# Kernel optimization log

Measured on AMD Instinct MI355X. Metric: run time of the kernel, lower is better.

The kernel has to match this reference:

```python
import jax, jax.numpy as jnp
import numpy as np

E = 32  # embedding_dim
B = 1048576

def setup_inputs() -> dict:
    key = jax.random.key(0)
    ks = jax.random.split(key, 16)
    def p(k, shape, scale=0.1):
        return jax.random.normal(k, shape, dtype=jnp.float32) * scale
    return {
        'x': jax.random.normal(ks[0], (B, 2, 5), dtype=jnp.float32),
        'fc_emb_w': p(ks[1], (E, 5)), 'fc_emb_b': p(ks[2], (E,)),
        'in_proj_w': p(ks[3], (3 * E, E)), 'in_proj_b': p(ks[4], (3 * E,)),
        'out_proj_w': p(ks[5], (E, E)), 'out_proj_b': p(ks[6], (E,)),
        'w_ih': p(ks[7], (E, E)), 'b_ih': p(ks[8], (E,)),
        'w_hh': p(ks[9], (E, E)), 'b_hh': p(ks[10], (E,)),
        'fc_dec_w': p(ks[11], (5, E)), 'fc_dec_b': p(ks[12], (5,)),
        'out_w': p(ks[13], (3, 5)), 'out_b': p(ks[14], (3,)),
    }

def gelu(x):
    return jax.nn.gelu(x, approximate=False)  # torch nn.GELU default (erf)

def reference(x, fc_emb_w, fc_emb_b, in_proj_w, in_proj_b,
              out_proj_w, out_proj_b, w_ih, b_ih, w_hh, b_hh,
              fc_dec_w, fc_dec_b, out_w, out_b):
    # per-token embedding: [B,2,5] -> [B,2,E]
    e = gelu(jnp.einsum('bsi,ei->bse', x, fc_emb_w) + fc_emb_b)
    # single-head self-attention (seq_len=2)
    wq, wk, wv = jnp.split(in_proj_w, 3, axis=0)
    bq, bk, bv = jnp.split(in_proj_b, 3, axis=0)
    q = jnp.einsum('bsd,ed->bse', e, wq) + bq
    k = jnp.einsum('bsd,ed->bse', e, wk) + bk
    v = jnp.einsum('bsd,ed->bse', e, wv) + bv
    scores = jnp.einsum('bqd,bkd->bqk', q, k) / jnp.sqrt(jnp.float32(E))
    attn = jax.nn.softmax(scores, axis=-1)
    o = jnp.einsum('bqk,bkd->bqd', attn, v)
    o = jnp.einsum('bsd,ed->bse', o, out_proj_w) + out_proj_b
    # 2-step tanh RNN, h0 = 0; final hidden state only
    h1 = jnp.tanh(o[:, 0] @ w_ih.T + b_ih + b_hh)
    h2 = jnp.tanh(o[:, 1] @ w_ih.T + b_ih + h1 @ w_hh.T + b_hh)
    # decode
    d = gelu(h2 @ fc_dec_w.T + fc_dec_b)
    return d @ out_w.T + out_b  # [B,3]
```

## Files before the change

kernel.cpp:

```cpp
#include <hip/hip_runtime.h>
#include <math.h>

#define BT 256

typedef _Float16 half2v __attribute__((ext_vector_type(2)));
typedef __fp16   fp16x2 __attribute__((ext_vector_type(2)));
typedef _Float16 half8  __attribute__((ext_vector_type(8)));
typedef float    f32x16 __attribute__((ext_vector_type(16)));

union U4H8 { unsigned int u[4]; half8 h; };
struct __attribute__((packed)) F3 { float a, b, c; };

__device__ __forceinline__ half2v u2h(unsigned int u){
  union { unsigned int u; half2v h; } c; c.u = u; return c.h;
}
__device__ __forceinline__ unsigned int h2u(half2v h){
  union { unsigned int u; half2v h; } c; c.h = h; return c.u;
}
__device__ __forceinline__ half2v pkrtz(float a, float b){
  union { fp16x2 f; half2v h; } c;
  c.f = __builtin_amdgcn_cvt_pkrtz(a, b);
  return c.h;
}
__device__ __forceinline__ float fdot2(half2v a, half2v b, float c){
  return __builtin_amdgcn_fdot2(a, b, c, false);
}
__device__ __forceinline__ float frcp(float x){ return __builtin_amdgcn_rcpf(x); }

__device__ __forceinline__ unsigned int pk_rne(float a, float b){
  half2v h; h.x = (_Float16)a; h.y = (_Float16)b; return h2u(h);
}

#if __has_builtin(__builtin_amdgcn_permlane32_swap)
#define HAVE_PLSWAP 1
#endif

__device__ __forceinline__ float red_sum32(float v){
#ifdef HAVE_PLSWAP
  union { float f; unsigned u; } c; c.f = v;
  auto r = __builtin_amdgcn_permlane32_swap(c.u, c.u, false, false);
  union { unsigned u; float f; } a, b; a.u = r[0]; b.u = r[1];
  return a.f + b.f;
#else
  return v + __shfl_xor(v, 32);
#endif
}
__device__ __forceinline__ float upper_to_lower(float v){
#ifdef HAVE_PLSWAP
  union { float f; unsigned u; } c; c.f = v;
  auto r = __builtin_amdgcn_permlane32_swap(c.u, c.u, false, false);
  union { unsigned u; float f; } b; b.u = r[1];
  return b.f;
#else
  return __shfl_xor(v, 32);
#endif
}
__device__ __forceinline__ float lower_to_upper(float v){
#ifdef HAVE_PLSWAP
  union { float f; unsigned u; } c; c.f = v;
  auto r = __builtin_amdgcn_permlane32_swap(c.u, c.u, false, false);
  union { unsigned u; float f; } a; a.u = r[0];
  return a.f;
#else
  return __shfl_xor(v, 32);
#endif
}

__device__ __forceinline__ half2v gelu_pk(half2v x){
  const _Float16 a0 = (_Float16)0.3989423f,  a1 = (_Float16)-0.0663157f,
                 a2 = (_Float16)0.0096298f,  a3 = (_Float16)-0.00095967f,
                 a4 = (_Float16)0.000048f,   hp = (_Float16)0.5f,
                 hn = (_Float16)-0.5f;
  const half2v A0={a0,a0}, A1={a1,a1}, A2={a2,a2}, A3={a3,a3}, A4={a4,a4};
  const half2v HP={hp,hp}, HN={hn,hn};
  half2v t = x*x;
  half2v q = A4*t + A3;
  q = q*t + A2;
  q = q*t + A1;
  q = q*t + A0;
  half2v u = x*q;
#if __has_builtin(__builtin_elementwise_min)
  u = __builtin_elementwise_max(u, HN);
  u = __builtin_elementwise_min(u, HP);
#else
  u.x = u.x > hp ? hp : (u.x < hn ? hn : u.x);
  u.y = u.y > hp ? hp : (u.y < hn ? hn : u.y);
#endif
  return x*(u + HP);
}

__device__ __forceinline__ half2v tanh_pk(half2v x){
  const _Float16 c0=(_Float16)0.999716f,  c1=(_Float16)-0.328107f,
                 c2=(_Float16)0.116352f,  c3=(_Float16)-0.031255f,
                 c4=(_Float16)0.005038f,  c5=(_Float16)-0.000348f,
                 tp=(_Float16)2.0f,       tn=(_Float16)-2.0f;
  const half2v C0={c0,c0},C1={c1,c1},C2={c2,c2},C3={c3,c3},C4={c4,c4},C5={c5,c5};
  const half2v TP={tp,tp}, TN={tn,tn};
#if __has_builtin(__builtin_elementwise_min)
  x = __builtin_elementwise_max(x, TN);
  x = __builtin_elementwise_min(x, TP);
#else
  x.x = x.x > tp ? tp : (x.x < tn ? tn : x.x);
  x.y = x.y > tp ? tp : (x.y < tn ? tn : x.y);
#endif
  half2v t = x*x;
  half2v p = C5*t + C4;
  p = p*t + C3;
  p = p*t + C2;
  p = p*t + C1;
  p = p*t + C0;
  return x*p;
}

__global__ void prep_kernel(const float* __restrict__ inw, const float* __restrict__ inb,
                            const float* __restrict__ opw, const float* __restrict__ opb,
                            const float* __restrict__ wih, const float* __restrict__ bih,
                            const float* __restrict__ bhh, const float* __restrict__ whh,
                            const float* __restrict__ decw, const float* __restrict__ embw,
                            const float* __restrict__ embb,
                            const float* __restrict__ decb, const float* __restrict__ outw,
                            unsigned int* __restrict__ wsu){
  __shared__ float sQ[1024], sK[1024], sV[1024], sOP[1024], sWI[1024];
  __shared__ float sA[1024], sP[1024], sM[1024], sT[32], sWV[32];
  const float ISS = 0.17677669529663689f;
  int t = threadIdx.x;
  sQ[t]  = inw[t];
  sK[t]  = inw[1024 + t];
  sV[t]  = inw[2048 + t];
  sOP[t] = opw[t];
  sWI[t] = wih[t];
  __syncthreads();
  int tx = t & 31, ty = t >> 5;
  float accA = 0.f, accP = 0.f;
  #pragma unroll
  for (int m = 0; m < 32; m++){
    accA += sQ[m*32 + ty] * sK[m*32 + tx];
    accP += sOP[ty*32 + m] * sV[m*32 + tx];
  }
  sA[ty*32 + tx] = accA;
  sP[ty*32 + tx] = accP;
  if (ty == 0){
    float aw = 0.f;
    #pragma unroll
    for (int m = 0; m < 32; m++) aw += inb[m] * sK[m*32 + tx];
    sWV[tx] = aw;
  }
  if (ty == 1){
    float at = opb[tx];
    #pragma unroll
    for (int m = 0; m < 32; m++) at += sOP[tx*32 + m] * inb[64 + m];
    sT[tx] = at;
  }
  __syncthreads();
  float accM = 0.f;
  #pragma unroll
  for (int m = 0; m < 32; m++) accM += sWI[ty*32 + m] * sP[m*32 + tx];
  sM[ty*32 + tx] = accM;
  if (ty == 2){
    float ab = bih[tx] + bhh[tx];
    #pragma unroll
    for (int m = 0; m < 32; m++) ab += sWI[tx*32 + m] * sT[m];
    ((float*)wsu)[2320 + tx] = ab;
  }
  __syncthreads();
  if (t < 512){
    int r = t >> 4, j = t & 15;
    int c0 = 16*(j>>3) + 8*((j>>1)&1) + 4*((j>>2)&1) + 2*(j&1);
    wsu[t]        = pk_rne(ISS*sA[r*32+c0], ISS*sA[r*32+c0+1]);
    wsu[512 + t]  = pk_rne(sM[r*32+c0],  sM[r*32+c0+1]);
    wsu[1024 + t] = pk_rne(whh[r*32+c0], whh[r*32+c0+1]);
    wsu[1536 + t] = (r < 5) ? pk_rne(decw[r*32+c0], decw[r*32+c0+1]) : 0u;
  } else if (t < 768){
    int q = t - 512, j2 = q >> 3, cc = (q & 7)*2;
    float a = (cc   < 5) ? embw[j2*5+cc]   : 0.f;
    float b = (cc+1 < 5) ? embw[j2*5+cc+1] : ((cc+1 == 5) ? embb[j2] : 0.f);
    wsu[2048 + q] = pk_rne(a, b);
  } else if (t < 784){
    int q = t - 768, gg = q >> 3, j = q & 7;
    int r0 = 2*(j&1) + 8*(j>>1) + 4*gg;
    wsu[2304 + q] = pk_rne(ISS*sWV[r0], ISS*sWV[r0+1]);
  } else if (t < 787){
    int i = t - 784, c = 2*i;
    float a = decb[c];
    float b = (c+1 < 5) ? decb[c+1] : 0.f;
    wsu[2352 + i] = pk_rne(a, b);
  } else if (t < 796){
    int q = t - 787;
    int r = (q >= 6) ? 2 : ((q >= 3) ? 1 : 0);
    int p = q - r*3, c = 2*p;
    float a = outw[r*5 + c];
    float b = (c+1 < 5) ? outw[r*5 + c + 1] : 0.f;
    wsu[2355 + q] = pk_rne(a, b);
  }
}

__device__ __forceinline__ half8 ldfrag(const unsigned int* __restrict__ p){
  U4H8 t; t.u[0]=p[0]; t.u[1]=p[1]; t.u[2]=p[2]; t.u[3]=p[3]; return t.h;
}
__device__ __forceinline__ half8 h8of(const unsigned int* q){
  U4H8 t; t.u[0]=q[0]; t.u[1]=q[1]; t.u[2]=q[2]; t.u[3]=q[3]; return t.h;
}

__device__ __forceinline__ f32x16 ldbias(const float* __restrict__ p, int grp){
  const float4* b = (const float4*)(p + 4*grp);
  float4 q0 = b[0], q1 = b[2], q2 = b[4], q3 = b[6];
  f32x16 c;
  c[0]=q0.x; c[1]=q0.y; c[2]=q0.z; c[3]=q0.w;
  c[4]=q1.x; c[5]=q1.y; c[6]=q1.z; c[7]=q1.w;
  c[8]=q2.x; c[9]=q2.y; c[10]=q2.z; c[11]=q2.w;
  c[12]=q3.x; c[13]=q3.y; c[14]=q3.z; c[15]=q3.w;
  return c;
}

__global__ __launch_bounds__(BT, 4) void fused_kernel(
    const float* __restrict__ x,
    const unsigned int* __restrict__ wsu,
    const float* __restrict__ outb,
    float* __restrict__ y, long long B)
{
  int tid  = threadIdx.x;
  int lane = tid & 63;
  int col  = lane & 31;
  bool g   = (lane >> 5) != 0;
  int grp  = g ? 1 : 0;

  unsigned B32  = (unsigned)B;
  unsigned Bm1  = B32 - 1u;
  unsigned eBase = ((unsigned)blockIdx.x*(BT/64) + (unsigned)(tid>>6)) * 64u;
  if (eBase >= B32) return;
  bool full = (eBase + 64u <= B32);

  const unsigned int* pA = wsu;
  const unsigned int* pM = wsu + 512;
  const unsigned int* pW = wsu + 1024;
  const unsigned int* pD = wsu + 1536;
  const unsigned int* pE = wsu + 2048;
  const unsigned int* pwv = wsu + 2304;
  const float* bMf = (const float*)(wsu + 2320);
  const unsigned int* pdb  = wsu + 2352;
  const unsigned int* pout = wsu + 2355;

  half8 embA = ldfrag(pE + col*8  + grp*4);
  half8 A1   = ldfrag(pA + col*16 + grp*4), A2 = ldfrag(pA + col*16 + 8 + grp*4);
  half8 M1   = ldfrag(pM + col*16 + grp*4), M2 = ldfrag(pM + col*16 + 8 + grp*4);
  half8 W1   = ldfrag(pW + col*16 + grp*4), W2 = ldfrag(pW + col*16 + 8 + grp*4);
  half8 D1   = ldfrag(pD + col*16 + grp*4), D2 = ldfrag(pD + col*16 + 8 + grp*4);
  half2v wv[8];
  #pragma unroll
  for (int j = 0; j < 8; j++) wv[j] = u2h(pwv[grp*8 + j]);
  unsigned db01u = pdb[0], db23u = pdb[1], db4u = pdb[2];

  f32x16 cb_bM = ldbias(bMf, grp);
  float ob0 = outb[0], ob1 = outb[1], ob2 = outb[2];
  f32x16 z16;
  #pragma unroll
  for (int i = 0; i < 16; i++) z16[i] = 0.f;

  U4H8 xb0[2], xb1[2];
  #pragma unroll
  for (int tt = 0; tt < 2; tt++){
    xb0[tt].u[0]=0u; xb0[tt].u[1]=0u; xb0[tt].u[2]=0u; xb0[tt].u[3]=0u;
    xb1[tt].u[0]=0u; xb1[tt].u[1]=0u; xb1[tt].u[2]=0u; xb1[tt].u[3]=0u;
  }
  if (!g){
    #pragma unroll
    for (int tt = 0; tt < 2; tt++){
      unsigned e = eBase + 32u*tt + (unsigned)col;
      e = e < Bm1 ? e : Bm1;
      const float2* xp = (const float2*)((const char*)x + (size_t)(e*40u));
      float2 p0 = xp[0], p1 = xp[1], p2 = xp[2], p3 = xp[3], p4 = xp[4];
      xb0[tt].u[0] = h2u(pkrtz(p0.x, p0.y));
      xb0[tt].u[1] = h2u(pkrtz(p1.x, p1.y));
      xb0[tt].u[2] = h2u(pkrtz(p2.x, 1.0f));
      xb1[tt].u[0] = h2u(pkrtz(p2.y, p3.x));
      xb1[tt].u[1] = h2u(pkrtz(p3.y, p4.x));
      xb1[tt].u[2] = h2u(pkrtz(p4.y, 1.0f));
    }
  }

  f32x16 e0D[2], e1D[2];
  #pragma unroll
  for (int tt = 0; tt < 2; tt++){
    e0D[tt] = __builtin_amdgcn_mfma_f32_32x32x16_f16(embA, xb0[tt].h, z16, 0,0,0);
    e1D[tt] = __builtin_amdgcn_mfma_f32_32x32x16_f16(embA, xb1[tt].h, z16, 0,0,0);
  }
  unsigned int epk[2][8], dlpk[2][8];
  #pragma unroll
  for (int tt = 0; tt < 2; tt++){
    #pragma unroll
    for (int i = 0; i < 8; i++){
      half2v e0h = gelu_pk(pkrtz(e0D[tt][2*i], e0D[tt][2*i+1]));
      half2v e1h = gelu_pk(pkrtz(e1D[tt][2*i], e1D[tt][2*i+1]));
      epk[tt][i]  = h2u(e0h);
      dlpk[tt][i] = h2u(e1h - e0h);
    }
  }

  f32x16 gD[2];
  #pragma unroll
  for (int tt = 0; tt < 2; tt++){
    gD[tt] = __builtin_amdgcn_mfma_f32_32x32x16_f16(A1, h8of(dlpk[tt]), z16, 0,0,0);
    gD[tt] = __builtin_amdgcn_mfma_f32_32x32x16_f16(A2, h8of(dlpk[tt]+4), gD[tt], 0,0,0);
  }
  float a01[2], a11[2];
  #pragma unroll
  for (int tt = 0; tt < 2; tt++){
    float t0 = 0.f, t1 = 0.f, dw = 0.f;
    #pragma unroll
    for (int i = 0; i < 8; i++){
      half2v gp = pkrtz(gD[tt][2*i], gD[tt][2*i+1]);
      t0 = fdot2(u2h(epk[tt][i]),  gp, t0);
      t1 = fdot2(u2h(dlpk[tt][i]), gp, t1);
      dw = fdot2(wv[i], u2h(dlpk[tt][i]), dw);
    }
    float s0 = red_sum32(t0 + dw);
    t1 = red_sum32(t1);
    a01[tt] = frcp(1.0f + __expf(-s0));
    a11[tt] = frcp(1.0f + __expf(-(s0 + t1)));
  }

  unsigned int c0pk[2][8], c1pk[2][8];
  #pragma unroll
  for (int tt = 0; tt < 2; tt++){
    _Float16 q01 = (_Float16)a01[tt], qda = (_Float16)(a11[tt] - a01[tt]);
    half2v s01 = {q01,q01}, sda = {qda,qda};
    #pragma unroll
    for (int j = 0; j < 8; j++){
      half2v c0 = u2h(dlpk[tt][j])*s01 + u2h(epk[tt][j]);
      half2v c1 = u2h(dlpk[tt][j])*sda + c0;
      c0pk[tt][j] = h2u(c0); c1pk[tt][j] = h2u(c1);
    }
  }

  f32x16 h1D[2];
  #pragma unroll
  for (int tt = 0; tt < 2; tt++){
    h1D[tt] = __builtin_amdgcn_mfma_f32_32x32x16_f16(M1, h8of(c0pk[tt]), cb_bM, 0,0,0);
    h1D[tt] = __builtin_amdgcn_mfma_f32_32x32x16_f16(M2, h8of(c0pk[tt]+4), h1D[tt], 0,0,0);
  }
  unsigned int h1pk[2][8];
  #pragma unroll
  for (int tt = 0; tt < 2; tt++)
    #pragma unroll
    for (int i = 0; i < 8; i++)
      h1pk[tt][i] = h2u(tanh_pk(pkrtz(h1D[tt][2*i], h1D[tt][2*i+1])));

  f32x16 h2D[2];
  #pragma unroll
  for (int tt = 0; tt < 2; tt++){
    h2D[tt] = __builtin_amdgcn_mfma_f32_32x32x16_f16(M1, h8of(c1pk[tt]), cb_bM, 0,0,0);
    h2D[tt] = __builtin_amdgcn_mfma_f32_32x32x16_f16(M2, h8of(c1pk[tt]+4), h2D[tt], 0,0,0);
    h2D[tt] = __builtin_amdgcn_mfma_f32_32x32x16_f16(W1, h8of(h1pk[tt]),   h2D[tt], 0,0,0);
    h2D[tt] = __builtin_amdgcn_mfma_f32_32x32x16_f16(W2, h8of(h1pk[tt]+4), h2D[tt], 0,0,0);
  }
  unsigned int h2pk[2][8];
  #pragma unroll
  for (int tt = 0; tt < 2; tt++)
    #pragma unroll
    for (int i = 0; i < 8; i++)
      h2pk[tt][i] = h2u(tanh_pk(pkrtz(h2D[tt][2*i], h2D[tt][2*i+1])));

  {
    half2v b01 = u2h(db01u), b23 = u2h(db23u), b4x = u2h(db4u);
    float db0 = (float)b01.x, db1 = (float)b01.y;
    float db2 = (float)b23.x, db3 = (float)b23.y;
    float db4 = (float)b4x.x;
    f32x16 cdec;
    #pragma unroll
    for (int i = 0; i < 16; i++) cdec[i] = 0.f;
    cdec[0] = g ? db4 : db0;
    cdec[1] = g ? 0.f : db1;
    cdec[2] = g ? 0.f : db2;
    cdec[3] = g ? 0.f : db3;

    f32x16 dvD[2];
    #pragma unroll
    for (int tt = 0; tt < 2; tt++){
      dvD[tt] = __builtin_amdgcn_mfma_f32_32x32x16_f16(D1, h8of(h2pk[tt]), cdec, 0,0,0);
      dvD[tt] = __builtin_amdgcn_mfma_f32_32x32x16_f16(D2, h8of(h2pk[tt]+4), dvD[tt], 0,0,0);
    }
    float d4l = upper_to_lower(dvD[0][0]);
    float q0  = lower_to_upper(dvD[1][0]);
    float q1  = lower_to_upper(dvD[1][1]);
    float q2  = lower_to_upper(dvD[1][2]);
    float q3  = lower_to_upper(dvD[1][3]);
    float d0 = g ? q0 : dvD[0][0];
    float d1 = g ? q1 : dvD[0][1];
    float d2 = g ? q2 : dvD[0][2];
    float d3 = g ? q3 : dvD[0][3];
    float d4 = g ? dvD[1][0] : d4l;
    half2v dp0 = gelu_pk(pkrtz(d0, d1));
    half2v dp1 = gelu_pk(pkrtz(d2, d3));
    half2v dp2 = gelu_pk(pkrtz(d4, 0.f));
    float y0 = fdot2(u2h(pout[0]), dp0, fdot2(u2h(pout[1]), dp1, fdot2(u2h(pout[2]), dp2, ob0)));
    float y1 = fdot2(u2h(pout[3]), dp0, fdot2(u2h(pout[4]), dp1, fdot2(u2h(pout[5]), dp2, ob1)));
    float y2 = fdot2(u2h(pout[6]), dp0, fdot2(u2h(pout[7]), dp1, fdot2(u2h(pout[8]), dp2, ob2)));
    unsigned e = eBase + (unsigned)lane;
    F3 out; out.a = y0; out.b = y1; out.c = y2;
    F3* yp = (F3*)((char*)y + (size_t)(e*12u));
    if (full){
      *yp = out;
    } else if (e < B32){
      *yp = out;
    }
  }
}

extern "C" void kernel_launch(void* const* d_in, const int* in_sizes, int n_in,
                              void* d_out, int out_size, void* d_ws, size_t ws_size,
                              hipStream_t stream){
  const float* x    = (const float*)d_in[0];
  const float* embw = (const float*)d_in[1];
  const float* embb = (const float*)d_in[2];
  const float* inw  = (const float*)d_in[3];
  const float* inb  = (const float*)d_in[4];
  const float* opw  = (const float*)d_in[5];
  const float* opb  = (const float*)d_in[6];
  const float* wih  = (const float*)d_in[7];
  const float* bih  = (const float*)d_in[8];
  const float* whh  = (const float*)d_in[9];
  const float* bhh  = (const float*)d_in[10];
  const float* decw = (const float*)d_in[11];
  const float* decb = (const float*)d_in[12];
  const float* outw = (const float*)d_in[13];
  const float* outb = (const float*)d_in[14];
  float* y = (float*)d_out;
  unsigned int* wsu = (unsigned int*)d_ws;

  long long B = in_sizes[0] / 10;
  long long elems_per_block = (BT/64) * 64;

  prep_kernel<<<1, 1024, 0, stream>>>(inw, inb, opw, opb, wih, bih, bhh,
                                      whh, decw, embw, embb, decb, outw, wsu);
  int grid = (int)((B + elems_per_block - 1)/elems_per_block);
  fused_kernel<<<grid, BT, 0, stream>>>(x, wsu, outb, y, B);
}
```

Measured before the change: 135.1 us.

## Process two 64-element tiles per wave, prefetching all inputs upfront

```diff
diff --git a/kernel.cpp b/kernel.cpp
--- a/kernel.cpp
+++ b/kernel.cpp
@@ -212,7 +212,7 @@
   return c;
 }
 
-__global__ __launch_bounds__(BT, 4) void fused_kernel(
+__global__ __launch_bounds__(BT, 3) void fused_kernel(
     const float* __restrict__ x,
     const unsigned int* __restrict__ wsu,
     const float* __restrict__ outb,
@@ -226,9 +226,8 @@
 
   unsigned B32  = (unsigned)B;
   unsigned Bm1  = B32 - 1u;
-  unsigned eBase = ((unsigned)blockIdx.x*(BT/64) + (unsigned)(tid>>6)) * 64u;
-  if (eBase >= B32) return;
-  bool full = (eBase + 64u <= B32);
+  unsigned eW = ((unsigned)blockIdx.x*(BT/64) + (unsigned)(tid>>6)) * 128u;
+  if (eW >= B32) return;
 
   const unsigned int* pA = wsu;
   const unsigned int* pM = wsu + 512;
@@ -256,152 +255,162 @@
   #pragma unroll
   for (int i = 0; i < 16; i++) z16[i] = 0.f;
 
-  U4H8 xb0[2], xb1[2];
-  #pragma unroll
-  for (int tt = 0; tt < 2; tt++){
-    xb0[tt].u[0]=0u; xb0[tt].u[1]=0u; xb0[tt].u[2]=0u; xb0[tt].u[3]=0u;
-    xb1[tt].u[0]=0u; xb1[tt].u[1]=0u; xb1[tt].u[2]=0u; xb1[tt].u[3]=0u;
+  U4H8 xb0[2][2], xb1[2][2];
+  #pragma unroll
+  for (int ps = 0; ps < 2; ps++){
+    #pragma unroll
+    for (int tt = 0; tt < 2; tt++){
+      xb0[ps][tt].u[0]=0u; xb0[ps][tt].u[1]=0u; xb0[ps][tt].u[2]=0u; xb0[ps][tt].u[3]=0u;
+      xb1[ps][tt].u[0]=0u; xb1[ps][tt].u[1]=0u; xb1[ps][tt].u[2]=0u; xb1[ps][tt].u[3]=0u;
+    }
   }
   if (!g){
     #pragma unroll
-    for (int tt = 0; tt < 2; tt++){
-      unsigned e = eBase + 32u*tt + (unsigned)col;
-      e = e < Bm1 ? e : Bm1;
-      const float2* xp = (const float2*)((const char*)x + (size_t)(e*40u));
-      float2 p0 = xp[0], p1 = xp[1], p2 = xp[2], p3 = xp[3], p4 = xp[4];
-      xb0[tt].u[0] = h2u(pkrtz(p0.x, p0.y));
-      xb0[tt].u[1] = h2u(pkrtz(p1.x, p1.y));
-      xb0[tt].u[2] = h2u(pkrtz(p2.x, 1.0f));
-      xb1[tt].u[0] = h2u(pkrtz(p2.y, p3.x));
-      xb1[tt].u[1] = h2u(pkrtz(p3.y, p4.x));
-      xb1[tt].u[2] = h2u(pkrtz(p4.y, 1.0f));
-    }
-  }
-
-  f32x16 e0D[2], e1D[2];
-  #pragma unroll
-  for (int tt = 0; tt < 2; tt++){
-    e0D[tt] = __builtin_amdgcn_mfma_f32_32x32x16_f16(embA, xb0[tt].h, z16, 0,0,0);
-    e1D[tt] = __builtin_amdgcn_mfma_f32_32x32x16_f16(embA, xb1[tt].h, z16, 0,0,0);
-  }
-  unsigned int epk[2][8], dlpk[2][8];
-  #pragma unroll
-  for (int tt = 0; tt < 2; tt++){
-    #pragma unroll
-    for (int i = 0; i < 8; i++){
-      half2v e0h = gelu_pk(pkrtz(e0D[tt][2*i], e0D[tt][2*i+1]));
-      half2v e1h = gelu_pk(pkrtz(e1D[tt][2*i], e1D[tt][2*i+1]));
-      epk[tt][i]  = h2u(e0h);
-      dlpk[tt][i] = h2u(e1h - e0h);
-    }
-  }
-
-  f32x16 gD[2];
-  #pragma unroll
-  for (int tt = 0; tt < 2; tt++){
-    gD[tt] = __builtin_amdgcn_mfma_f32_32x32x16_f16(A1, h8of(dlpk[tt]), z16, 0,0,0);
-    gD[tt] = __builtin_amdgcn_mfma_f32_32x32x16_f16(A2, h8of(dlpk[tt]+4), gD[tt], 0,0,0);
-  }
-  float a01[2], a11[2];
-  #pragma unroll
-  for (int tt = 0; tt < 2; tt++){
-    float t0 = 0.f, t1 = 0.f, dw = 0.f;
-    #pragma unroll
-    for (int i = 0; i < 8; i++){
-      half2v gp = pkrtz(gD[tt][2*i], gD[tt][2*i+1]);
-      t0 = fdot2(u2h(epk[tt][i]),  gp, t0);
-      t1 = fdot2(u2h(dlpk[tt][i]), gp, t1);
-      dw = fdot2(wv[i], u2h(dlpk[tt][i]), dw);
-    }
-    float s0 = red_sum32(t0 + dw);
-    t1 = red_sum32(t1);
-    a01[tt] = frcp(1.0f + __expf(-s0));
-    a11[tt] = frcp(1.0f + __expf(-(s0 + t1)));
-  }
-
-  unsigned int c0pk[2][8], c1pk[2][8];
-  #pragma unroll
-  for (int tt = 0; tt < 2; tt++){
-    _Float16 q01 = (_Float16)a01[tt], qda = (_Float16)(a11[tt] - a01[tt]);
-    half2v s01 = {q01,q01}, sda = {qda,qda};
-    #pragma unroll
-    for (int j = 0; j < 8; j++){
-      half2v c0 = u2h(dlpk[tt][j])*s01 + u2h(epk[tt][j]);
-      half2v c1 = u2h(dlpk[tt][j])*sda + c0;
-      c0pk[tt][j] = h2u(c0); c1pk[tt][j] = h2u(c1);
-    }
-  }
-
-  f32x16 h1D[2];
-  #pragma unroll
-  for (int tt = 0; tt < 2; tt++){
-    h1D[tt] = __builtin_amdgcn_mfma_f32_32x32x16_f16(M1, h8of(c0pk[tt]), cb_bM, 0,0,0);
-    h1D[tt] = __builtin_amdgcn_mfma_f32_32x32x16_f16(M2, h8of(c0pk[tt]+4), h1D[tt], 0,0,0);
-  }
-  unsigned int h1pk[2][8];
-  #pragma unroll
-  for (int tt = 0; tt < 2; tt++)
-    #pragma unroll
-    for (int i = 0; i < 8; i++)
-      h1pk[tt][i] = h2u(tanh_pk(pkrtz(h1D[tt][2*i], h1D[tt][2*i+1])));
-
-  f32x16 h2D[2];
-  #pragma unroll
-  for (int tt = 0; tt < 2; tt++){
-    h2D[tt] = __builtin_amdgcn_mfma_f32_32x32x16_f16(M1, h8of(c1pk[tt]), cb_bM, 0,0,0);
-    h2D[tt] = __builtin_amdgcn_mfma_f32_32x32x16_f16(M2, h8of(c1pk[tt]+4), h2D[tt], 0,0,0);
-    h2D[tt] = __builtin_amdgcn_mfma_f32_32x32x16_f16(W1, h8of(h1pk[tt]),   h2D[tt], 0,0,0);
-    h2D[tt] = __builtin_amdgcn_mfma_f32_32x32x16_f16(W2, h8of(h1pk[tt]+4), h2D[tt], 0,0,0);
-  }
-  unsigned int h2pk[2][8];
-  #pragma unroll
-  for (int tt = 0; tt < 2; tt++)
-    #pragma unroll
-    for (int i = 0; i < 8; i++)
-      h2pk[tt][i] = h2u(tanh_pk(pkrtz(h2D[tt][2*i], h2D[tt][2*i+1])));
-
-  {
-    half2v b01 = u2h(db01u), b23 = u2h(db23u), b4x = u2h(db4u);
-    float db0 = (float)b01.x, db1 = (float)b01.y;
-    float db2 = (float)b23.x, db3 = (float)b23.y;
-    float db4 = (float)b4x.x;
-    f32x16 cdec;
-    #pragma unroll
-    for (int i = 0; i < 16; i++) cdec[i] = 0.f;
-    cdec[0] = g ? db4 : db0;
-    cdec[1] = g ? 0.f : db1;
-    cdec[2] = g ? 0.f : db2;
-    cdec[3] = g ? 0.f : db3;
-
-    f32x16 dvD[2];
-    #pragma unroll
-    for (int tt = 0; tt < 2; tt++){
-      dvD[tt] = __builtin_amdgcn_mfma_f32_32x32x16_f16(D1, h8of(h2pk[tt]), cdec, 0,0,0);
-      dvD[tt] = __builtin_amdgcn_mfma_f32_32x32x16_f16(D2, h8of(h2pk[tt]+4), dvD[tt], 0,0,0);
-    }
-    float d4l = upper_to_lower(dvD[0][0]);
-    float q0  = lower_to_upper(dvD[1][0]);
-    float q1  = lower_to_upper(dvD[1][1]);
-    float q2  = lower_to_upper(dvD[1][2]);
-    float q3  = lower_to_upper(dvD[1][3]);
-    float d0 = g ? q0 : dvD[0][0];
-    float d1 = g ? q1 : dvD[0][1];
-    float d2 = g ? q2 : dvD[0][2];
-    float d3 = g ? q3 : dvD[0][3];
-    float d4 = g ? dvD[1][0] : d4l;
-    half2v dp0 = gelu_pk(pkrtz(d0, d1));
-    half2v dp1 = gelu_pk(pkrtz(d2, d3));
-    half2v dp2 = gelu_pk(pkrtz(d4, 0.f));
-    float y0 = fdot2(u2h(pout[0]), dp0, fdot2(u2h(pout[1]), dp1, fdot2(u2h(pout[2]), dp2, ob0)));
-    float y1 = fdot2(u2h(pout[3]), dp0, fdot2(u2h(pout[4]), dp1, fdot2(u2h(pout[5]), dp2, ob1)));
-    float y2 = fdot2(u2h(pout[6]), dp0, fdot2(u2h(pout[7]), dp1, fdot2(u2h(pout[8]), dp2, ob2)));
-    unsigned e = eBase + (unsigned)lane;
-    F3 out; out.a = y0; out.b = y1; out.c = y2;
-    F3* yp = (F3*)((char*)y + (size_t)(e*12u));
-    if (full){
-      *yp = out;
-    } else if (e < B32){
-      *yp = out;
+    for (int ps = 0; ps < 2; ps++){
+      #pragma unroll
+      for (int tt = 0; tt < 2; tt++){
+        unsigned e = eW + 64u*ps + 32u*tt + (unsigned)col;
+        e = e < Bm1 ? e : Bm1;
+        const float2* xp = (const float2*)((const char*)x + (size_t)(e*40u));
+        float2 p0 = xp[0], p1 = xp[1], p2 = xp[2], p3 = xp[3], p4 = xp[4];
+        xb0[ps][tt].u[0] = h2u(pkrtz(p0.x, p0.y));
+        xb0[ps][tt].u[1] = h2u(pkrtz(p1.x, p1.y));
+        xb0[ps][tt].u[2] = h2u(pkrtz(p2.x, 1.0f));
+        xb1[ps][tt].u[0] = h2u(pkrtz(p2.y, p3.x));
+        xb1[ps][tt].u[1] = h2u(pkrtz(p3.y, p4.x));
+        xb1[ps][tt].u[2] = h2u(pkrtz(p4.y, 1.0f));
+      }
+    }
+  }
+
+  #pragma unroll
+  for (int ps = 0; ps < 2; ps++){
+    if (ps == 1 && eW + 64u >= B32) break;
+    unsigned eB0 = eW + 64u*ps;
+
+    f32x16 e0D[2], e1D[2];
+    #pragma unroll
+    for (int tt = 0; tt < 2; tt++){
+      e0D[tt] = __builtin_amdgcn_mfma_f32_32x32x16_f16(embA, xb0[ps][tt].h, z16, 0,0,0);
+      e1D[tt] = __builtin_amdgcn_mfma_f32_32x32x16_f16(embA, xb1[ps][tt].h, z16, 0,0,0);
+    }
+    unsigned int epk[2][8], dlpk[2][8];
+    #pragma unroll
+    for (int tt = 0; tt < 2; tt++){
+      #pragma unroll
+      for (int i = 0; i < 8; i++){
+        half2v e0h = gelu_pk(pkrtz(e0D[tt][2*i], e0D[tt][2*i+1]));
+        half2v e1h = gelu_pk(pkrtz(e1D[tt][2*i], e1D[tt][2*i+1]));
+        epk[tt][i]  = h2u(e0h);
+        dlpk[tt][i] = h2u(e1h - e0h);
+      }
+    }
+
+    f32x16 gD[2];
+    #pragma unroll
+    for (int tt = 0; tt < 2; tt++){
+      gD[tt] = __builtin_amdgcn_mfma_f32_32x32x16_f16(A1, h8of(dlpk[tt]), z16, 0,0,0);
+      gD[tt] = __builtin_amdgcn_mfma_f32_32x32x16_f16(A2, h8of(dlpk[tt]+4), gD[tt], 0,0,0);
+    }
+    float a01[2], a11[2];
+    #pragma unroll
+    for (int tt = 0; tt < 2; tt++){
+      float t0 = 0.f, t1 = 0.f, dw = 0.f;
+      #pragma unroll
+      for (int i = 0; i < 8; i++){
+        half2v gp = pkrtz(gD[tt][2*i], gD[tt][2*i+1]);
+        t0 = fdot2(u2h(epk[tt][i]),  gp, t0);
+        t1 = fdot2(u2h(dlpk[tt][i]), gp, t1);
+        dw = fdot2(wv[i], u2h(dlpk[tt][i]), dw);
+      }
+      float s0 = red_sum32(t0 + dw);
+      t1 = red_sum32(t1);
+      a01[tt] = frcp(1.0f + __expf(-s0));
+      a11[tt] = frcp(1.0f + __expf(-(s0 + t1)));
+    }
+
+    unsigned int c0pk[2][8], c1pk[2][8];
+    #pragma unroll
+    for (int tt = 0; tt < 2; tt++){
+      _Float16 q01 = (_Float16)a01[tt], qda = (_Float16)(a11[tt] - a01[tt]);
+      half2v s01 = {q01,q01}, sda = {qda,qda};
+      #pragma unroll
+      for (int j = 0; j < 8; j++){
+        half2v c0 = u2h(dlpk[tt][j])*s01 + u2h(epk[tt][j]);
+        half2v c1 = u2h(dlpk[tt][j])*sda + c0;
+        c0pk[tt][j] = h2u(c0); c1pk[tt][j] = h2u(c1);
+      }
+    }
+
+    f32x16 h1D[2];
+    #pragma unroll
+    for (int tt = 0; tt < 2; tt++){
+      h1D[tt] = __builtin_amdgcn_mfma_f32_32x32x16_f16(M1, h8of(c0pk[tt]), cb_bM, 0,0,0);
+      h1D[tt] = __builtin_amdgcn_mfma_f32_32x32x16_f16(M2, h8of(c0pk[tt]+4), h1D[tt], 0,0,0);
+    }
+    unsigned int h1pk[2][8];
+    #pragma unroll
+    for (int tt = 0; tt < 2; tt++)
+      #pragma unroll
+      for (int i = 0; i < 8; i++)
+        h1pk[tt][i] = h2u(tanh_pk(pkrtz(h1D[tt][2*i], h1D[tt][2*i+1])));
+
+    f32x16 h2D[2];
+    #pragma unroll
+    for (int tt = 0; tt < 2; tt++){
+      h2D[tt] = __builtin_amdgcn_mfma_f32_32x32x16_f16(M1, h8of(c1pk[tt]), cb_bM, 0,0,0);
+      h2D[tt] = __builtin_amdgcn_mfma_f32_32x32x16_f16(M2, h8of(c1pk[tt]+4), h2D[tt], 0,0,0);
+      h2D[tt] = __builtin_amdgcn_mfma_f32_32x32x16_f16(W1, h8of(h1pk[tt]),   h2D[tt], 0,0,0);
+      h2D[tt] = __builtin_amdgcn_mfma_f32_32x32x16_f16(W2, h8of(h1pk[tt]+4), h2D[tt], 0,0,0);
+    }
+    unsigned int h2pk[2][8];
+    #pragma unroll
+    for (int tt = 0; tt < 2; tt++)
+      #pragma unroll
+      for (int i = 0; i < 8; i++)
+        h2pk[tt][i] = h2u(tanh_pk(pkrtz(h2D[tt][2*i], h2D[tt][2*i+1])));
+
+    {
+      half2v b01 = u2h(db01u), b23 = u2h(db23u), b4x = u2h(db4u);
+      float db0 = (float)b01.x, db1 = (float)b01.y;
+      float db2 = (float)b23.x, db3 = (float)b23.y;
+      float db4 = (float)b4x.x;
+      f32x16 cdec;
+      #pragma unroll
+      for (int i = 0; i < 16; i++) cdec[i] = 0.f;
+      cdec[0] = g ? db4 : db0;
+      cdec[1] = g ? 0.f : db1;
+      cdec[2] = g ? 0.f : db2;
+      cdec[3] = g ? 0.f : db3;
+
+      f32x16 dvD[2];
+      #pragma unroll
+      for (int tt = 0; tt < 2; tt++){
+        dvD[tt] = __builtin_amdgcn_mfma_f32_32x32x16_f16(D1, h8of(h2pk[tt]), cdec, 0,0,0);
+        dvD[tt] = __builtin_amdgcn_mfma_f32_32x32x16_f16(D2, h8of(h2pk[tt]+4), dvD[tt], 0,0,0);
+      }
+      float d4l = upper_to_lower(dvD[0][0]);
+      float q0  = lower_to_upper(dvD[1][0]);
+      float q1  = lower_to_upper(dvD[1][1]);
+      float q2  = lower_to_upper(dvD[1][2]);
+      float q3  = lower_to_upper(dvD[1][3]);
+      float d0 = g ? q0 : dvD[0][0];
+      float d1 = g ? q1 : dvD[0][1];
+      float d2 = g ? q2 : dvD[0][2];
+      float d3 = g ? q3 : dvD[0][3];
+      float d4 = g ? dvD[1][0] : d4l;
+      half2v dp0 = gelu_pk(pkrtz(d0, d1));
+      half2v dp1 = gelu_pk(pkrtz(d2, d3));
+      half2v dp2 = gelu_pk(pkrtz(d4, 0.f));
+      float y0 = fdot2(u2h(pout[0]), dp0, fdot2(u2h(pout[1]), dp1, fdot2(u2h(pout[2]), dp2, ob0)));
+      float y1 = fdot2(u2h(pout[3]), dp0, fdot2(u2h(pout[4]), dp1, fdot2(u2h(pout[5]), dp2, ob1)));
+      float y2 = fdot2(u2h(pout[6]), dp0, fdot2(u2h(pout[7]), dp1, fdot2(u2h(pout[8]), dp2, ob2)));
+      unsigned e = eB0 + (unsigned)lane;
+      if (e < B32){
+        F3 out; out.a = y0; out.b = y1; out.c = y2;
+        F3* yp = (F3*)((char*)y + (size_t)(e*12u));
+        *yp = out;
+      }
     }
   }
 }
@@ -428,7 +437,7 @@
   unsigned int* wsu = (unsigned int*)d_ws;
 
   long long B = in_sizes[0] / 10;
-  long long elems_per_block = (BT/64) * 64;
+  long long elems_per_block = (BT/64) * 128;
 
   prep_kernel<<<1, 1024, 0, stream>>>(inw, inb, opw, opb, wih, bih, bhh,
                                       whh, decw, embw, embb, decb, outw, wsu);
```

Result: no change. 135.9 us (+0.6%).

## Process 128 elements per wave with four MFMA tiles and deferred weight loads

Applied to the files above, without the earlier changes.

```diff
diff --git a/kernel.cpp b/kernel.cpp
--- a/kernel.cpp
+++ b/kernel.cpp
@@ -212,7 +212,7 @@
   return c;
 }
 
-__global__ __launch_bounds__(BT, 4) void fused_kernel(
+__global__ __launch_bounds__(BT, 2) void fused_kernel(
     const float* __restrict__ x,
     const unsigned int* __restrict__ wsu,
     const float* __restrict__ outb,
@@ -226,9 +226,8 @@
 
   unsigned B32  = (unsigned)B;
   unsigned Bm1  = B32 - 1u;
-  unsigned eBase = ((unsigned)blockIdx.x*(BT/64) + (unsigned)(tid>>6)) * 64u;
-  if (eBase >= B32) return;
-  bool full = (eBase + 64u <= B32);
+  unsigned eW = ((unsigned)blockIdx.x*(BT/64) + (unsigned)(tid>>6)) * 128u;
+  if (eW >= B32) return;
 
   const unsigned int* pA = wsu;
   const unsigned int* pM = wsu + 512;
@@ -243,29 +242,25 @@
   half8 embA = ldfrag(pE + col*8  + grp*4);
   half8 A1   = ldfrag(pA + col*16 + grp*4), A2 = ldfrag(pA + col*16 + 8 + grp*4);
   half8 M1   = ldfrag(pM + col*16 + grp*4), M2 = ldfrag(pM + col*16 + 8 + grp*4);
-  half8 W1   = ldfrag(pW + col*16 + grp*4), W2 = ldfrag(pW + col*16 + 8 + grp*4);
-  half8 D1   = ldfrag(pD + col*16 + grp*4), D2 = ldfrag(pD + col*16 + 8 + grp*4);
   half2v wv[8];
   #pragma unroll
   for (int j = 0; j < 8; j++) wv[j] = u2h(pwv[grp*8 + j]);
-  unsigned db01u = pdb[0], db23u = pdb[1], db4u = pdb[2];
 
   f32x16 cb_bM = ldbias(bMf, grp);
-  float ob0 = outb[0], ob1 = outb[1], ob2 = outb[2];
   f32x16 z16;
   #pragma unroll
   for (int i = 0; i < 16; i++) z16[i] = 0.f;
 
-  U4H8 xb0[2], xb1[2];
-  #pragma unroll
-  for (int tt = 0; tt < 2; tt++){
+  U4H8 xb0[4], xb1[4];
+  #pragma unroll
+  for (int tt = 0; tt < 4; tt++){
     xb0[tt].u[0]=0u; xb0[tt].u[1]=0u; xb0[tt].u[2]=0u; xb0[tt].u[3]=0u;
     xb1[tt].u[0]=0u; xb1[tt].u[1]=0u; xb1[tt].u[2]=0u; xb1[tt].u[3]=0u;
   }
   if (!g){
     #pragma unroll
-    for (int tt = 0; tt < 2; tt++){
-      unsigned e = eBase + 32u*tt + (unsigned)col;
+    for (int tt = 0; tt < 4; tt++){
+      unsigned e = eW + 32u*tt + (unsigned)col;
       e = e < Bm1 ? e : Bm1;
       const float2* xp = (const float2*)((const char*)x + (size_t)(e*40u));
       float2 p0 = xp[0], p1 = xp[1], p2 = xp[2], p3 = xp[3], p4 = xp[4];
@@ -278,90 +273,103 @@
     }
   }
 
-  f32x16 e0D[2], e1D[2];
-  #pragma unroll
-  for (int tt = 0; tt < 2; tt++){
-    e0D[tt] = __builtin_amdgcn_mfma_f32_32x32x16_f16(embA, xb0[tt].h, z16, 0,0,0);
-    e1D[tt] = __builtin_amdgcn_mfma_f32_32x32x16_f16(embA, xb1[tt].h, z16, 0,0,0);
-  }
-  unsigned int epk[2][8], dlpk[2][8];
-  #pragma unroll
-  for (int tt = 0; tt < 2; tt++){
-    #pragma unroll
-    for (int i = 0; i < 8; i++){
-      half2v e0h = gelu_pk(pkrtz(e0D[tt][2*i], e0D[tt][2*i+1]));
-      half2v e1h = gelu_pk(pkrtz(e1D[tt][2*i], e1D[tt][2*i+1]));
-      epk[tt][i]  = h2u(e0h);
-      dlpk[tt][i] = h2u(e1h - e0h);
-    }
-  }
-
-  f32x16 gD[2];
-  #pragma unroll
-  for (int tt = 0; tt < 2; tt++){
-    gD[tt] = __builtin_amdgcn_mfma_f32_32x32x16_f16(A1, h8of(dlpk[tt]), z16, 0,0,0);
-    gD[tt] = __builtin_amdgcn_mfma_f32_32x32x16_f16(A2, h8of(dlpk[tt]+4), gD[tt], 0,0,0);
-  }
-  float a01[2], a11[2];
-  #pragma unroll
-  for (int tt = 0; tt < 2; tt++){
-    float t0 = 0.f, t1 = 0.f, dw = 0.f;
-    #pragma unroll
-    for (int i = 0; i < 8; i++){
-      half2v gp = pkrtz(gD[tt][2*i], gD[tt][2*i+1]);
-      t0 = fdot2(u2h(epk[tt][i]),  gp, t0);
-      t1 = fdot2(u2h(dlpk[tt][i]), gp, t1);
-      dw = fdot2(wv[i], u2h(dlpk[tt][i]), dw);
-    }
-    float s0 = red_sum32(t0 + dw);
-    t1 = red_sum32(t1);
-    a01[tt] = frcp(1.0f + __expf(-s0));
-    a11[tt] = frcp(1.0f + __expf(-(s0 + t1)));
-  }
-
-  unsigned int c0pk[2][8], c1pk[2][8];
-  #pragma unroll
-  for (int tt = 0; tt < 2; tt++){
+  unsigned int epk[4][8], dlpk[4][8];
+  #pragma unroll
+  for (int pr = 0; pr < 2; pr++){
+    f32x16 e0D[2], e1D[2];
+    #pragma unroll
+    for (int q = 0; q < 2; q++){
+      int tt = pr*2 + q;
+      e0D[q] = __builtin_amdgcn_mfma_f32_32x32x16_f16(embA, xb0[tt].h, z16, 0,0,0);
+      e1D[q] = __builtin_amdgcn_mfma_f32_32x32x16_f16(embA, xb1[tt].h, z16, 0,0,0);
+    }
+    #pragma unroll
+    for (int q = 0; q < 2; q++){
+      int tt = pr*2 + q;
+      #pragma unroll
+      for (int i = 0; i < 8; i++){
+        half2v e0h = gelu_pk(pkrtz(e0D[q][2*i], e0D[q][2*i+1]));
+        half2v e1h = gelu_pk(pkrtz(e1D[q][2*i], e1D[q][2*i+1]));
+        epk[tt][i]  = h2u(e0h);
+        dlpk[tt][i] = h2u(e1h - e0h);
+      }
+    }
+  }
+
+  float a01[4], a11[4];
+  {
+    f32x16 gD[4];
+    #pragma unroll
+    for (int tt = 0; tt < 4; tt++){
+      gD[tt] = __builtin_amdgcn_mfma_f32_32x32x16_f16(A1, h8of(dlpk[tt]), z16, 0,0,0);
+      gD[tt] = __builtin_amdgcn_mfma_f32_32x32x16_f16(A2, h8of(dlpk[tt]+4), gD[tt], 0,0,0);
+    }
+    #pragma unroll
+    for (int tt = 0; tt < 4; tt++){
+      float t0 = 0.f, t1 = 0.f, dw = 0.f;
+      #pragma unroll
+      for (int i = 0; i < 8; i++){
+        half2v gp = pkrtz(gD[tt][2*i], gD[tt][2*i+1]);
+        t0 = fdot2(u2h(epk[tt][i]),  gp, t0);
+        t1 = fdot2(u2h(dlpk[tt][i]), gp, t1);
+        dw = fdot2(wv[i], u2h(dlpk[tt][i]), dw);
+      }
+      float s0 = red_sum32(t0 + dw);
+      t1 = red_sum32(t1);
+      a01[tt] = frcp(1.0f + __expf(-s0));
+      a11[tt] = frcp(1.0f + __expf(-(s0 + t1)));
+    }
+  }
+
+  #pragma unroll
+  for (int tt = 0; tt < 4; tt++){
     _Float16 q01 = (_Float16)a01[tt], qda = (_Float16)(a11[tt] - a01[tt]);
     half2v s01 = {q01,q01}, sda = {qda,qda};
     #pragma unroll
     for (int j = 0; j < 8; j++){
       half2v c0 = u2h(dlpk[tt][j])*s01 + u2h(epk[tt][j]);
       half2v c1 = u2h(dlpk[tt][j])*sda + c0;
-      c0pk[tt][j] = h2u(c0); c1pk[tt][j] = h2u(c1);
-    }
-  }
-
-  f32x16 h1D[2];
-  #pragma unroll
-  for (int tt = 0; tt < 2; tt++){
-    h1D[tt] = __builtin_amdgcn_mfma_f32_32x32x16_f16(M1, h8of(c0pk[tt]), cb_bM, 0,0,0);
-    h1D[tt] = __builtin_amdgcn_mfma_f32_32x32x16_f16(M2, h8of(c0pk[tt]+4), h1D[tt], 0,0,0);
-  }
-  unsigned int h1pk[2][8];
-  #pragma unroll
-  for (int tt = 0; tt < 2; tt++)
-    #pragma unroll
-    for (int i = 0; i < 8; i++)
-      h1pk[tt][i] = h2u(tanh_pk(pkrtz(h1D[tt][2*i], h1D[tt][2*i+1])));
-
-  f32x16 h2D[2];
-  #pragma unroll
-  for (int tt = 0; tt < 2; tt++){
-    h2D[tt] = __builtin_amdgcn_mfma_f32_32x32x16_f16(M1, h8of(c1pk[tt]), cb_bM, 0,0,0);
-    h2D[tt] = __builtin_amdgcn_mfma_f32_32x32x16_f16(M2, h8of(c1pk[tt]+4), h2D[tt], 0,0,0);
-    h2D[tt] = __builtin_amdgcn_mfma_f32_32x32x16_f16(W1, h8of(h1pk[tt]),   h2D[tt], 0,0,0);
-    h2D[tt] = __builtin_amdgcn_mfma_f32_32x32x16_f16(W2, h8of(h1pk[tt]+4), h2D[tt], 0,0,0);
-  }
-  unsigned int h2pk[2][8];
-  #pragma unroll
-  for (int tt = 0; tt < 2; tt++)
-    #pragma unroll
-    for (int i = 0; i < 8; i++)
-      h2pk[tt][i] = h2u(tanh_pk(pkrtz(h2D[tt][2*i], h2D[tt][2*i+1])));
-
+      epk[tt][j]  = h2u(c0);
+      dlpk[tt][j] = h2u(c1);
+    }
+  }
+
+  unsigned int h1pk[4][8];
   {
-    half2v b01 = u2h(db01u), b23 = u2h(db23u), b4x = u2h(db4u);
+    f32x16 h1D[4];
+    #pragma unroll
+    for (int tt = 0; tt < 4; tt++){
+      h1D[tt] = __builtin_amdgcn_mfma_f32_32x32x16_f16(M1, h8of(epk[tt]), cb_bM, 0,0,0);
+      h1D[tt] = __builtin_amdgcn_mfma_f32_32x32x16_f16(M2, h8of(epk[tt]+4), h1D[tt], 0,0,0);
+    }
+    #pragma unroll
+    for (int tt = 0; tt < 4; tt++)
+      #pragma unroll
+      for (int i = 0; i < 8; i++)
+        h1pk[tt][i] = h2u(tanh_pk(pkrtz(h1D[tt][2*i], h1D[tt][2*i+1])));
+  }
+
+  unsigned int h2pk[4][8];
+  {
+    half8 W1 = ldfrag(pW + col*16 + grp*4), W2 = ldfrag(pW + col*16 + 8 + grp*4);
+    f32x16 h2D[4];
+    #pragma unroll
+    for (int tt = 0; tt < 4; tt++){
+      h2D[tt] = __builtin_amdgcn_mfma_f32_32x32x16_f16(M1, h8of(dlpk[tt]), cb_bM, 0,0,0);
+      h2D[tt] = __builtin_amdgcn_mfma_f32_32x32x16_f16(M2, h8of(dlpk[tt]+4), h2D[tt], 0,0,0);
+      h2D[tt] = __builtin_amdgcn_mfma_f32_32x32x16_f16(W1, h8of(h1pk[tt]),   h2D[tt], 0,0,0);
+      h2D[tt] = __builtin_amdgcn_mfma_f32_32x32x16_f16(W2, h8of(h1pk[tt]+4), h2D[tt], 0,0,0);
+    }
+    #pragma unroll
+    for (int tt = 0; tt < 4; tt++)
+      #pragma unroll
+      for (int i = 0; i < 8; i++)
+        h2pk[tt][i] = h2u(tanh_pk(pkrtz(h2D[tt][2*i], h2D[tt][2*i+1])));
+  }
+
+  {
+    half8 D1 = ldfrag(pD + col*16 + grp*4), D2 = ldfrag(pD + col*16 + 8 + grp*4);
+    half2v b01 = u2h(pdb[0]), b23 = u2h(pdb[1]), b4x = u2h(pdb[2]);
     float db0 = (float)b01.x, db1 = (float)b01.y;
     float db2 = (float)b23.x, db3 = (float)b23.y;
     float db4 = (float)b4x.x;
@@ -372,36 +380,39 @@
     cdec[1] = g ? 0.f : db1;
     cdec[2] = g ? 0.f : db2;
     cdec[3] = g ? 0.f : db3;
-
-    f32x16 dvD[2];
-    #pragma unroll
-    for (int tt = 0; tt < 2; tt++){
+    float ob0 = outb[0], ob1 = outb[1], ob2 = outb[2];
+
+    f32x16 dvD[4];
+    #pragma unroll
+    for (int tt = 0; tt < 4; tt++){
       dvD[tt] = __builtin_amdgcn_mfma_f32_32x32x16_f16(D1, h8of(h2pk[tt]), cdec, 0,0,0);
       dvD[tt] = __builtin_amdgcn_mfma_f32_32x32x16_f16(D2, h8of(h2pk[tt]+4), dvD[tt], 0,0,0);
     }
-    float d4l = upper_to_lower(dvD[0][0]);
-    float q0  = lower_to_upper(dvD[1][0]);
-    float q1  = lower_to_upper(dvD[1][1]);
-    float q2  = lower_to_upper(dvD[1][2]);
-    float q3  = lower_to_upper(dvD[1][3]);
-    float d0 = g ? q0 : dvD[0][0];
-    float d1 = g ? q1 : dvD[0][1];
-    float d2 = g ? q2 : dvD[0][2];
-    float d3 = g ? q3 : dvD[0][3];
-    float d4 = g ? dvD[1][0] : d4l;
-    half2v dp0 = gelu_pk(pkrtz(d0, d1));
-    half2v dp1 = gelu_pk(pkrtz(d2, d3));
-    half2v dp2 = gelu_pk(pkrtz(d4, 0.f));
-    float y0 = fdot2(u2h(pout[0]), dp0, fdot2(u2h(pout[1]), dp1, fdot2(u2h(pout[2]), dp2, ob0)));
-    float y1 = fdot2(u2h(pout[3]), dp0, fdot2(u2h(pout[4]), dp1, fdot2(u2h(pout[5]), dp2, ob1)));
-    float y2 = fdot2(u2h(pout[6]), dp0, fdot2(u2h(pout[7]), dp1, fdot2(u2h(pout[8]), dp2, ob2)));
-    unsigned e = eBase + (unsigned)lane;
-    F3 out; out.a = y0; out.b = y1; out.c = y2;
-    F3* yp = (F3*)((char*)y + (size_t)(e*12u));
-    if (full){
-      *yp = out;
-    } else if (e < B32){
-      *yp = out;
+    #pragma unroll
+    for (int p = 0; p < 2; p++){
+      int lo = 2*p, hi = 2*p + 1;
+      float d4l = upper_to_lower(dvD[lo][0]);
+      float q0  = lower_to_upper(dvD[hi][0]);
+      float q1  = lower_to_upper(dvD[hi][1]);
+      float q2  = lower_to_upper(dvD[hi][2]);
+      float q3  = lower_to_upper(dvD[hi][3]);
+      float d0 = g ? q0 : dvD[lo][0];
+      float d1 = g ? q1 : dvD[lo][1];
+      float d2 = g ? q2 : dvD[lo][2];
+      float d3 = g ? q3 : dvD[lo][3];
+      float d4 = g ? dvD[hi][0] : d4l;
+      half2v dp0 = gelu_pk(pkrtz(d0, d1));
+      half2v dp1 = gelu_pk(pkrtz(d2, d3));
+      half2v dp2 = gelu_pk(pkrtz(d4, 0.f));
+      float y0 = fdot2(u2h(pout[0]), dp0, fdot2(u2h(pout[1]), dp1, fdot2(u2h(pout[2]), dp2, ob0)));
+      float y1 = fdot2(u2h(pout[3]), dp0, fdot2(u2h(pout[4]), dp1, fdot2(u2h(pout[5]), dp2, ob1)));
+      float y2 = fdot2(u2h(pout[6]), dp0, fdot2(u2h(pout[7]), dp1, fdot2(u2h(pout[8]), dp2, ob2)));
+      unsigned e = eW + 64u*p + (unsigned)lane;
+      if (e < B32){
+        F3 out; out.a = y0; out.b = y1; out.c = y2;
+        F3* yp = (F3*)((char*)y + (size_t)(e*12u));
+        *yp = out;
+      }
     }
   }
 }
@@ -428,7 +439,7 @@
   unsigned int* wsu = (unsigned int*)d_ws;
 
   long long B = in_sizes[0] / 10;
-  long long elems_per_block = (BT/64) * 64;
+  long long elems_per_block = (BT/64) * 128;
 
   prep_kernel<<<1, 1024, 0, stream>>>(inw, inb, opw, opb, wih, bih, bhh,
                                       whh, decw, embw, embb, decb, outw, wsu);
```

New measurement: 141.4 us. 4.7% more time.
